# Performance work log

Hardware: AMD Instinct MI355X
Metric: run time of the kernel (lower is better)

Reference implementation:

```python
import jax, jax.numpy as jnp
import numpy as np

B, Q, V, H = 8, 128, 512, 512


def setup_inputs() -> dict:
    key = jax.random.key(0)
    ks = jax.random.split(key, 6)
    s = 1.0 / np.sqrt(H)
    return {
        "query": jax.random.normal(ks[0], (B, Q, H), jnp.float32),
        "values": jax.random.normal(ks[1], (B, V, H), jnp.float32),
        "mask": jax.random.randint(ks[2], (B, V), 0, 2, jnp.int32),
        "Wq": jax.random.normal(ks[3], (H, H), jnp.float32) * s,
        "bq": jnp.zeros((H,), jnp.float32),
        "Wv": jax.random.normal(ks[4], (H, H), jnp.float32) * s,
        "bv": jnp.zeros((H,), jnp.float32),
        "wc": jax.random.normal(ks[5], (H, 1), jnp.float32) * s,
        "bc": jnp.zeros((1,), jnp.float32),
    }


def reference(query, values, mask, Wq, bq, Wv, bv, wc, bc):
    # Project once per token (Q*H and V*H GEMMs), then broadcast-add:
    # faithful to tanh(Lq(q)[:, :, None] + Lv(v)[:, None]) since Linear is
    # applied along the last dim and broadcasting commutes with it.
    qp = jnp.einsum('bqh,kh->bqk', query, Wq) + bq          # [B,Q,H]
    vp = jnp.einsum('bvh,kh->bvk', values, Wv) + bv          # [B,V,H]
    added = jnp.tanh(qp[:, :, None, :] + vp[:, None, :, :])  # [B,Q,V,H]
    scores = jnp.einsum('bqvh,ho->bqv', added, wc) + bc[0]   # [B,Q,V]
    neg_inf = jnp.array(-jnp.inf, scores.dtype)
    scores = jnp.where(mask[:, None, :] == 0, neg_inf, scores)
    weights = jax.nn.softmax(scores, axis=-1)                # [B,Q,V]
    context = jnp.einsum('bqv,bvh->bqh', weights, values)    # [B,Q,H]
    return (context, weights)
```

## Files before the change

### kernel.cpp

```cpp
#include <hip/hip_runtime.h>
#include <hip/hip_bf16.h>


#define C_SCALE 2.8853900817779268f

typedef __attribute__((ext_vector_type(8))) short short8;
typedef __attribute__((ext_vector_type(4))) float f32x4;
typedef __attribute__((ext_vector_type(2))) float f32x2;

__device__ __forceinline__ float fexp2(float x) { return __builtin_amdgcn_exp2f(x); }
__device__ __forceinline__ float frcp(float x)  { return __builtin_amdgcn_rcpf(x); }

__device__ __forceinline__ void bf_split(float x, short& hi, short& lo) {
  unsigned u = __builtin_bit_cast(unsigned, x);
  unsigned r = u + 0x7fffu + ((u >> 16) & 1u);
  hi = (short)(r >> 16);
  float hf = __builtin_bit_cast(float, r & 0xffff0000u);
  lo = (short)(__builtin_bit_cast(unsigned, x - hf) >> 16);
}

__global__ __launch_bounds__(256) void proj_gemm_mfma(
    const float* __restrict__ query, const float* __restrict__ values,
    const float* __restrict__ Wq, const float* __restrict__ Wv,
    const float* __restrict__ bq, const float* __restrict__ bv,
    float* __restrict__ qp, float* __restrict__ vp)
{
  __shared__ short sAhi[64 * 72];
  __shared__ short sAlo[64 * 72];
  __shared__ short sWhi[64 * 72];
  __shared__ short sWlo[64 * 72];

  const int t    = threadIdx.x;
  const int lane = t & 63;
  const int w    = t >> 6;
  const int by   = blockIdx.y;
  const bool isQ = (by < 16);
  const float* A    = isQ ? query : values;
  const float* W    = isQ ? Wq : Wv;
  const float* bias = isQ ? bq : bv;
  float*       out  = isQ ? qp : vp;
  const int m0 = (isQ ? by : (by - 16)) << 6;
  const int n0 = blockIdx.x << 6;

  const int srow = t >> 2, scol = t & 3;
  const float* Ap = A + (size_t)(m0 + srow) * 512 + (scol << 2);
  const float* Wp = W + (size_t)(n0 + srow) * 512 + (scol << 2);

  const int mw = (w & 1) << 5, nw = (w >> 1) << 5;
  const int frow = lane & 15, fquad = lane >> 4;

  f32x4 acc[2][2] = {};
  float4 pfA[4], pfW[4];
#pragma unroll
  for (int p = 0; p < 4; ++p) {
    pfA[p] = *(const float4*)(Ap + (p << 4));
    pfW[p] = *(const float4*)(Wp + (p << 4));
  }

  for (int kc = 0; kc < 512; kc += 64) {
    __syncthreads();
#pragma unroll
    for (int p = 0; p < 4; ++p) {
      float av[4] = {pfA[p].x, pfA[p].y, pfA[p].z, pfA[p].w};
      float wv[4] = {pfW[p].x, pfW[p].y, pfW[p].z, pfW[p].w};
      short4 ah, al, wh, wl;
      short* ahp = (short*)&ah; short* alp = (short*)&al;
      short* whp = (short*)&wh; short* wlp = (short*)&wl;
#pragma unroll
      for (int k = 0; k < 4; ++k) {
        bf_split(av[k], ahp[k], alp[k]);
        bf_split(wv[k], whp[k], wlp[k]);
      }
      const int ofs = srow * 72 + ((p << 2) + scol) * 4;
      *(short4*)&sAhi[ofs] = ah; *(short4*)&sAlo[ofs] = al;
      *(short4*)&sWhi[ofs] = wh; *(short4*)&sWlo[ofs] = wl;
    }
    __syncthreads();
    if (kc + 64 < 512) {
#pragma unroll
      for (int p = 0; p < 4; ++p) {
        pfA[p] = *(const float4*)(Ap + kc + 64 + (p << 4));
        pfW[p] = *(const float4*)(Wp + kc + 64 + (p << 4));
      }
    }
#pragma unroll
    for (int kb = 0; kb < 2; ++kb) {
      const int ko = kb * 32 + fquad * 8;
      short8 ahi[2], alo[2], whi[2], wlo[2];
#pragma unroll
      for (int mt = 0; mt < 2; ++mt) {
        const int r = (mw + mt * 16 + frow) * 72 + ko;
        ahi[mt] = *(const short8*)&sAhi[r];
        alo[mt] = *(const short8*)&sAlo[r];
      }
#pragma unroll
      for (int nt = 0; nt < 2; ++nt) {
        const int r = (nw + nt * 16 + frow) * 72 + ko;
        whi[nt] = *(const short8*)&sWhi[r];
        wlo[nt] = *(const short8*)&sWlo[r];
      }
#pragma unroll
      for (int mt = 0; mt < 2; ++mt)
#pragma unroll
        for (int nt = 0; nt < 2; ++nt) {
          acc[mt][nt] = __builtin_amdgcn_mfma_f32_16x16x32_bf16(
              alo[mt], whi[nt], acc[mt][nt], 0, 0, 0);
          acc[mt][nt] = __builtin_amdgcn_mfma_f32_16x16x32_bf16(
              ahi[mt], wlo[nt], acc[mt][nt], 0, 0, 0);
          acc[mt][nt] = __builtin_amdgcn_mfma_f32_16x16x32_bf16(
              ahi[mt], whi[nt], acc[mt][nt], 0, 0, 0);
        }
    }
  }

#pragma unroll
  for (int nt = 0; nt < 2; ++nt) {
    const int n = n0 + nw + nt * 16 + frow;
    const float bn = bias[n];
#pragma unroll
    for (int mt = 0; mt < 2; ++mt) {
      float vreg[4] = {acc[mt][nt].x, acc[mt][nt].y, acc[mt][nt].z, acc[mt][nt].w};
#pragma unroll
      for (int r = 0; r < 4; ++r) {
        const int m = m0 + mw + mt * 16 + fquad * 4 + r;
        out[(size_t)m * 512 + n] = fexp2(C_SCALE * (vreg[r] + bn));
      }
    }
  }
}

template<int NU>
__device__ __forceinline__ void score_chunkC(
    const float* __restrict__ vpb,
    const f32x2 (&Eq0a)[8][2], const f32x2 (&Eq1a)[8][2], const f32x2 (&wca)[8][2],
    const int* idxs, float* __restrict__ ow0,
    int s00, int i0, int hi, int c4, int lane)
{
  int su[NU];
  unsigned voff[NU];
  f32x2 a0[NU], a1[NU];
#pragma unroll
  for (int u = 0; u < NU; ++u) {
    su[u] = s00 + ((i0 + u) << 4);
    voff[u] = ((unsigned)idxs[su[u] & 511] << 9) + (unsigned)c4;
    a0[u] = (f32x2){0.f, 0.f}; a1[u] = (f32x2){0.f, 0.f};
  }
  const f32x2 one2 = {1.f, 1.f};
#pragma unroll
  for (int j = 0; j < 8; ++j) {
    float4 vv[NU];
#pragma unroll
    for (int u = 0; u < NU; ++u)
      vv[u] = *(const float4*)(vpb + voff[u] + (unsigned)(j << 6));
#pragma unroll
    for (int u = 0; u < NU; ++u) {
      const f32x2 Ev[2] = {{vv[u].x, vv[u].y}, {vv[u].z, vv[u].w}};
#pragma unroll
      for (int kp = 0; kp < 2; ++kp) {
        f32x2 e0 = Ev[kp] * Eq0a[j][kp];
        f32x2 e1 = Ev[kp] * Eq1a[j][kp];
        f32x2 d0 = e0 + one2;
        f32x2 d1 = e1 + one2;
        f32x2 pr = d0 * d1;
        f32x2 P  = {frcp(pr.x), frcp(pr.y)};
        a0[u] = __builtin_elementwise_fma(wca[j][kp] * d1, P, a0[u]);
        a1[u] = __builtin_elementwise_fma(wca[j][kp] * d0, P, a1[u]);
      }
    }
  }
#pragma unroll
  for (int u = 0; u < NU; ++u) {
    float s0 = a0[u].x + a0[u].y;
    float s1 = a1[u].x + a1[u].y;
#pragma unroll
    for (int off = 1; off < 16; off <<= 1) {
      s0 += __shfl_xor(s0, off, 64);
      s1 += __shfl_xor(s1, off, 64);
    }
    if (su[u] < hi && (lane & 15) == (i0 + u)) {
      ow0[su[u]]       = s0;
      ow0[512 + su[u]] = s1;
    }
  }
}

__global__ __launch_bounds__(256) void attn_score(
    const float* __restrict__ qp, const float* __restrict__ vp,
    const int* __restrict__ mask, const float* __restrict__ wc,
    float* __restrict__ out_w)
{
  __shared__ int idxs[512];
  __shared__ int cnt8[8];

  const int t    = threadIdx.x;
  const int lane = t & 63;
  const int w    = t >> 6;
  const int b    = blockIdx.x & 7;
  const int qg   = blockIdx.x >> 3;
  const int rowbase = b * 128 + qg * 2;

  idxs[t] = 0; idxs[t + 256] = 0;
  const int mv0 = mask[b * 512 + t];
  const int mv1 = mask[b * 512 + 256 + t];
  const unsigned long long bal0 = __ballot(mv0 != 0);
  const unsigned long long bal1 = __ballot(mv1 != 0);
  if (lane == 0) { cnt8[w] = __popcll(bal0); cnt8[w + 4] = __popcll(bal1); }
  __syncthreads();
  int cnt = 0, off0 = 0, off4 = 0;
#pragma unroll
  for (int j = 0; j < 8; ++j) {
    if (j == w)     off0 = cnt;
    if (j == w + 4) off4 = cnt;
    cnt += cnt8[j];
  }
  if (mv0) idxs[off0 + __popcll(bal0 & ((1ull << lane) - 1ull))] = t;
  if (mv1) idxs[off4 + __popcll(bal1 & ((1ull << lane) - 1ull))] = t + 256;
  __syncthreads();

  const int c  = blockIdx.y;
  const int lo = (cnt * c) >> 2;
  const int hi = (cnt * (c + 1)) >> 2;
  const int NI = (hi - lo + 15) >> 4;
  const int g  = lane >> 4;
  const int c4 = (lane & 15) << 2;
  const int s00 = lo + (w << 2) + g;

  const float* vpb = vp + (size_t)b * 512 * 512;
  const float* qr0 = qp + (size_t)rowbase * 512;
  float* ow0 = out_w + (size_t)rowbase * 512;

  f32x2 Eq0a[8][2], Eq1a[8][2], wca[8][2];
#pragma unroll
  for (int j = 0; j < 8; ++j) {
    const int hoff = (j << 6) + c4;
    const float4 q0v = *(const float4*)(qr0 + hoff);
    const float4 q1v = *(const float4*)(qr0 + 512 + hoff);
    const float4 wcv = *(const float4*)(wc + hoff);
    Eq0a[j][0] = (f32x2){q0v.x, q0v.y}; Eq0a[j][1] = (f32x2){q0v.z, q0v.w};
    Eq1a[j][0] = (f32x2){q1v.x, q1v.y}; Eq1a[j][1] = (f32x2){q1v.z, q1v.w};
    wca[j][0]  = (f32x2){wcv.x, wcv.y}; wca[j][1]  = (f32x2){wcv.z, wcv.w};
  }

  int i0 = 0;
  for (; i0 + 4 <= NI; i0 += 4)
    score_chunkC<4>(vpb, Eq0a, Eq1a, wca, idxs, ow0, s00, i0, hi, c4, lane);
  for (; i0 < NI; ++i0)
    score_chunkC<1>(vpb, Eq0a, Eq1a, wca, idxs, ow0, s00, i0, hi, c4, lane);
}

__global__ __launch_bounds__(512) void attn_finish(
    const float* __restrict__ values, const int* __restrict__ mask,
    float* __restrict__ out_ctx, float* __restrict__ out_w)
{
  __shared__ int   idxs[512];
  __shared__ float wls2[512][2];
  __shared__ int   cnt8[8];

  const int t    = threadIdx.x;
  const int lane = t & 63;
  const int w    = t >> 6;
  const int b    = blockIdx.x & 7;
  const int qg   = blockIdx.x >> 3;
  const int rowbase = b * 128 + qg * 2;

  ((float*)wls2)[t]       = 0.f;
  ((float*)wls2)[t + 512] = 0.f;
  idxs[t] = 0;
  const int mv = mask[b * 512 + t];
  const unsigned long long bal = __ballot(mv != 0);
  if (lane == 0) cnt8[w] = __popcll(bal);
  __syncthreads();
  int cnt = 0, offw = 0;
#pragma unroll
  for (int j = 0; j < 8; ++j) { if (j == w) offw = cnt; cnt += cnt8[j]; }
  int iinv = -1;
  if (mv) {
    iinv = offw + __popcll(bal & ((1ull << lane) - 1ull));
    idxs[iinv] = t;
  }
  __syncthreads();

  {
    const int mq = (w >= 4) ? 1 : 0;
    const float* srow = out_w + (size_t)(rowbase + mq) * 512;
    float4 u0 = ((const float4*)srow)[lane * 2];
    float4 u1 = ((const float4*)srow)[lane * 2 + 1];
    float s8[8] = {u0.x, u0.y, u0.z, u0.w, u1.x, u1.y, u1.z, u1.w};
#pragma unroll
    for (int k = 0; k < 8; ++k)
      if (lane * 8 + k >= cnt) s8[k] = 3.4e38f;
    float m = s8[0];
#pragma unroll
    for (int k = 1; k < 8; ++k) m = fminf(m, s8[k]);
#pragma unroll
    for (int off = 1; off < 64; off <<= 1) m = fminf(m, __shfl_xor(m, off, 64));
    float e[8], S = 0.f;
#pragma unroll
    for (int k = 0; k < 8; ++k) { e[k] = fexp2(C_SCALE * (m - s8[k])); S += e[k]; }
#pragma unroll
    for (int off = 1; off < 64; off <<= 1) S += __shfl_xor(S, off, 64);
    const float rinv = frcp(S);
    if (w == 0 || w == 4) {
#pragma unroll
      for (int k = 0; k < 8; ++k) {
        const int s = lane * 8 + k;
        if (s < cnt) wls2[s][mq] = e[k] * rinv;
      }
    }
  }
  __syncthreads();

  {
    float w0 = 0.f, w1 = 0.f;
    if (iinv >= 0) { w0 = wls2[iinv][0]; w1 = wls2[iinv][1]; }
    out_w[(size_t)rowbase * 512 + t]       = w0;
    out_w[(size_t)(rowbase + 1) * 512 + t] = w1;
  }

  const int NC = (cnt + 3) >> 2;
  const int g  = lane >> 4;
  const int c4 = (lane & 15) << 2;
  const unsigned hbase = (unsigned)(w * 64 + c4);
  const float* vb = values + (size_t)b * 512 * 512;
  float c0[4] = {0.f, 0.f, 0.f, 0.f}, c1[4] = {0.f, 0.f, 0.f, 0.f};
#pragma unroll 4
  for (int i = 0; i < NC; ++i) {
    const int s = (i << 2) + g;
    const unsigned ro = ((unsigned)idxs[s] << 9) + hbase;
    const float2 wg = *(const float2*)&wls2[s][0];
    const float4 v4 = *(const float4*)(vb + ro);
    float vv[4] = {v4.x, v4.y, v4.z, v4.w};
#pragma unroll
    for (int k = 0; k < 4; ++k) {
      c0[k] = __builtin_fmaf(wg.x, vv[k], c0[k]);
      c1[k] = __builtin_fmaf(wg.y, vv[k], c1[k]);
    }
  }
#pragma unroll
  for (int k = 0; k < 4; ++k) {
    c0[k] += __shfl_xor(c0[k], 16, 64); c0[k] += __shfl_xor(c0[k], 32, 64);
    c1[k] += __shfl_xor(c1[k], 16, 64); c1[k] += __shfl_xor(c1[k], 32, 64);
  }
  if (lane < 16) {
    float4 o0 = {c0[0], c0[1], c0[2], c0[3]};
    float4 o1 = {c1[0], c1[1], c1[2], c1[3]};
    *(float4*)(out_ctx + (size_t)rowbase * 512 + w * 64 + lane * 4)       = o0;
    *(float4*)(out_ctx + (size_t)(rowbase + 1) * 512 + w * 64 + lane * 4) = o1;
  }
}

extern "C" void kernel_launch(void* const* d_in, const int* in_sizes, int n_in,
                              void* d_out, int out_size, void* d_ws, size_t ws_size,
                              hipStream_t stream) {
  const float* query  = (const float*)d_in[0];
  const float* values = (const float*)d_in[1];
  const int*   mask   = (const int*)d_in[2];
  const float* Wq     = (const float*)d_in[3];
  const float* bq     = (const float*)d_in[4];
  const float* Wv     = (const float*)d_in[5];
  const float* bv     = (const float*)d_in[6];
  const float* wc     = (const float*)d_in[7];

  float* out   = (float*)d_out;
  float* out_w = out + (size_t)8 * 128 * 512;
  float* qp    = (float*)d_ws;
  float* vp    = qp + (size_t)1024 * 512;

  proj_gemm_mfma<<<dim3(8, 80), 256, 0, stream>>>(query, values, Wq, Wv, bq, bv, qp, vp);
  attn_score<<<dim3(512, 4), 256, 0, stream>>>(qp, vp, mask, wc, out_w);
  attn_finish<<<512, 512, 0, stream>>>(values, mask, out, out_w);
}
```

Measured before the change: 137.1 us.

## Fuse softmax/context finish into score kernel via last-block atomic counter

After: 323.3 us. 136% more time.

```diff
diff --git a/kernel.cpp b/kernel.cpp
--- a/kernel.cpp
+++ b/kernel.cpp
@@ -23,7 +23,8 @@
     const float* __restrict__ query, const float* __restrict__ values,
     const float* __restrict__ Wq, const float* __restrict__ Wv,
     const float* __restrict__ bq, const float* __restrict__ bv,
-    float* __restrict__ qp, float* __restrict__ vp)
+    float* __restrict__ qp, float* __restrict__ vp,
+    float* __restrict__ out_ctx)
 {
   __shared__ short sAhi[64 * 72];
   __shared__ short sAlo[64 * 72];
@@ -34,6 +35,16 @@
   const int lane = t & 63;
   const int w    = t >> 6;
   const int by   = blockIdx.y;
+
+  if (blockIdx.x == 0 && by == 0) {
+#pragma unroll
+    for (int i = 0; i < 2; ++i) {
+      const int q = t + i * 256;
+      const int bb = q >> 6, qg = q & 63;
+      ((int*)out_ctx)[(size_t)(bb * 128 + qg * 2) * 512] = 0;
+    }
+  }
+
   const bool isQ = (by < 16);
   const float* A    = isQ ? query : values;
   const float* W    = isQ ? Wq : Wv;
@@ -184,13 +195,16 @@
   }
 }
 
-__global__ __launch_bounds__(256) void attn_score(
+__global__ __launch_bounds__(256) void attn_score_finish(
     const float* __restrict__ qp, const float* __restrict__ vp,
-    const int* __restrict__ mask, const float* __restrict__ wc,
-    float* __restrict__ out_w)
+    const float* __restrict__ values, const int* __restrict__ mask,
+    const float* __restrict__ wc,
+    float* __restrict__ out_ctx, float* __restrict__ out_w)
 {
-  __shared__ int idxs[512];
-  __shared__ int cnt8[8];
+  __shared__ int   idxs[512];
+  __shared__ int   cnt8[8];
+  __shared__ float wls2[512][2];
+  __shared__ int   isLast;
 
   const int t    = threadIdx.x;
   const int lane = t & 63;
@@ -199,6 +213,10 @@
   const int qg   = blockIdx.x >> 3;
   const int rowbase = b * 128 + qg * 2;
 
+  ((float*)wls2)[t]       = 0.f;
+  ((float*)wls2)[t + 256] = 0.f;
+  ((float*)wls2)[t + 512] = 0.f;
+  ((float*)wls2)[t + 768] = 0.f;
   idxs[t] = 0; idxs[t + 256] = 0;
   const int mv0 = mask[b * 512 + t];
   const int mv1 = mask[b * 512 + 256 + t];
@@ -213,8 +231,9 @@
     if (j == w + 4) off4 = cnt;
     cnt += cnt8[j];
   }
-  if (mv0) idxs[off0 + __popcll(bal0 & ((1ull << lane) - 1ull))] = t;
-  if (mv1) idxs[off4 + __popcll(bal1 & ((1ull << lane) - 1ull))] = t + 256;
+  int iinv0 = -1, iinv1 = -1;
+  if (mv0) { iinv0 = off0 + __popcll(bal0 & ((1ull << lane) - 1ull)); idxs[iinv0] = t; }
+  if (mv1) { iinv1 = off4 + __popcll(bal1 & ((1ull << lane) - 1ull)); idxs[iinv1] = t + 256; }
   __syncthreads();
 
   const int c  = blockIdx.y;
@@ -246,42 +265,19 @@
     score_chunkC<4>(vpb, Eq0a, Eq1a, wca, idxs, ow0, s00, i0, hi, c4, lane);
   for (; i0 < NI; ++i0)
     score_chunkC<1>(vpb, Eq0a, Eq1a, wca, idxs, ow0, s00, i0, hi, c4, lane);
-}
-
-__global__ __launch_bounds__(512) void attn_finish(
-    const float* __restrict__ values, const int* __restrict__ mask,
-    float* __restrict__ out_ctx, float* __restrict__ out_w)
-{
-  __shared__ int   idxs[512];
-  __shared__ float wls2[512][2];
-  __shared__ int   cnt8[8];
-
-  const int t    = threadIdx.x;
-  const int lane = t & 63;
-  const int w    = t >> 6;
-  const int b    = blockIdx.x & 7;
-  const int qg   = blockIdx.x >> 3;
-  const int rowbase = b * 128 + qg * 2;
-
-  ((float*)wls2)[t]       = 0.f;
-  ((float*)wls2)[t + 512] = 0.f;
-  idxs[t] = 0;
-  const int mv = mask[b * 512 + t];
-  const unsigned long long bal = __ballot(mv != 0);
-  if (lane == 0) cnt8[w] = __popcll(bal);
-  __syncthreads();
-  int cnt = 0, offw = 0;
-#pragma unroll
-  for (int j = 0; j < 8; ++j) { if (j == w) offw = cnt; cnt += cnt8[j]; }
-  int iinv = -1;
-  if (mv) {
-    iinv = offw + __popcll(bal & ((1ull << lane) - 1ull));
-    idxs[iinv] = t;
-  }
-  __syncthreads();
+
+  __threadfence();
+  __syncthreads();
+  if (t == 0) {
+    int old = atomicAdd((int*)(out_ctx + (size_t)rowbase * 512), 1);
+    isLast = (old == 3) ? 1 : 0;
+  }
+  __syncthreads();
+  if (!isLast) return;
+  __threadfence();
 
   {
-    const int mq = (w >= 4) ? 1 : 0;
+    const int mq = w >> 1;
     const float* srow = out_w + (size_t)(rowbase + mq) * 512;
     float4 u0 = ((const float4*)srow)[lane * 2];
     float4 u1 = ((const float4*)srow)[lane * 2 + 1];
@@ -300,7 +296,7 @@
 #pragma unroll
     for (int off = 1; off < 64; off <<= 1) S += __shfl_xor(S, off, 64);
     const float rinv = frcp(S);
-    if (w == 0 || w == 4) {
+    if (w == 0 || w == 2) {
 #pragma unroll
       for (int k = 0; k < 8; ++k) {
         const int s = lane * 8 + k;
@@ -311,41 +307,55 @@
   __syncthreads();
 
   {
-    float w0 = 0.f, w1 = 0.f;
-    if (iinv >= 0) { w0 = wls2[iinv][0]; w1 = wls2[iinv][1]; }
-    out_w[(size_t)rowbase * 512 + t]       = w0;
-    out_w[(size_t)(rowbase + 1) * 512 + t] = w1;
+    float w00 = iinv0 >= 0 ? wls2[iinv0][0] : 0.f;
+    float w01 = iinv0 >= 0 ? wls2[iinv0][1] : 0.f;
+    float w10 = iinv1 >= 0 ? wls2[iinv1][0] : 0.f;
+    float w11 = iinv1 >= 0 ? wls2[iinv1][1] : 0.f;
+    out_w[(size_t)rowbase * 512 + t]             = w00;
+    out_w[(size_t)(rowbase + 1) * 512 + t]       = w01;
+    out_w[(size_t)rowbase * 512 + 256 + t]       = w10;
+    out_w[(size_t)(rowbase + 1) * 512 + 256 + t] = w11;
   }
 
   const int NC = (cnt + 3) >> 2;
-  const int g  = lane >> 4;
-  const int c4 = (lane & 15) << 2;
-  const unsigned hbase = (unsigned)(w * 64 + c4);
+  const unsigned hb0 = (unsigned)(w * 128 + c4);
   const float* vb = values + (size_t)b * 512 * 512;
-  float c0[4] = {0.f, 0.f, 0.f, 0.f}, c1[4] = {0.f, 0.f, 0.f, 0.f};
+  float c00[4] = {}, c01[4] = {}, c10[4] = {}, c11[4] = {};
 #pragma unroll 4
   for (int i = 0; i < NC; ++i) {
     const int s = (i << 2) + g;
-    const unsigned ro = ((unsigned)idxs[s] << 9) + hbase;
+    const unsigned ro = ((unsigned)idxs[s] << 9);
     const float2 wg = *(const float2*)&wls2[s][0];
-    const float4 v4 = *(const float4*)(vb + ro);
-    float vv[4] = {v4.x, v4.y, v4.z, v4.w};
+    const float4 v0 = *(const float4*)(vb + ro + hb0);
+    const float4 v1 = *(const float4*)(vb + ro + hb0 + 64);
+    const float a0[4] = {v0.x, v0.y, v0.z, v0.w};
+    const float a1[4] = {v1.x, v1.y, v1.z, v1.w};
 #pragma unroll
     for (int k = 0; k < 4; ++k) {
-      c0[k] = __builtin_fmaf(wg.x, vv[k], c0[k]);
-      c1[k] = __builtin_fmaf(wg.y, vv[k], c1[k]);
+      c00[k] = __builtin_fmaf(wg.x, a0[k], c00[k]);
+      c01[k] = __builtin_fmaf(wg.x, a1[k], c01[k]);
+      c10[k] = __builtin_fmaf(wg.y, a0[k], c10[k]);
+      c11[k] = __builtin_fmaf(wg.y, a1[k], c11[k]);
     }
   }
 #pragma unroll
   for (int k = 0; k < 4; ++k) {
-    c0[k] += __shfl_xor(c0[k], 16, 64); c0[k] += __shfl_xor(c0[k], 32, 64);
-    c1[k] += __shfl_xor(c1[k], 16, 64); c1[k] += __shfl_xor(c1[k], 32, 64);
+    c00[k] += __shfl_xor(c00[k], 16, 64); c00[k] += __shfl_xor(c00[k], 32, 64);
+    c01[k] += __shfl_xor(c01[k], 16, 64); c01[k] += __shfl_xor(c01[k], 32, 64);
+    c10[k] += __shfl_xor(c10[k], 16, 64); c10[k] += __shfl_xor(c10[k], 32, 64);
+    c11[k] += __shfl_xor(c11[k], 16, 64); c11[k] += __shfl_xor(c11[k], 32, 64);
   }
   if (lane < 16) {
-    float4 o0 = {c0[0], c0[1], c0[2], c0[3]};
-    float4 o1 = {c1[0], c1[1], c1[2], c1[3]};
-    *(float4*)(out_ctx + (size_t)rowbase * 512 + w * 64 + lane * 4)       = o0;
-    *(float4*)(out_ctx + (size_t)(rowbase + 1) * 512 + w * 64 + lane * 4) = o1;
+    float4 o00 = {c00[0], c00[1], c00[2], c00[3]};
+    float4 o01 = {c01[0], c01[1], c01[2], c01[3]};
+    float4 o10 = {c10[0], c10[1], c10[2], c10[3]};
+    float4 o11 = {c11[0], c11[1], c11[2], c11[3]};
+    float* r0 = out_ctx + (size_t)rowbase * 512;
+    float* r1 = out_ctx + (size_t)(rowbase + 1) * 512;
+    *(float4*)(r0 + hb0)      = o00;
+    *(float4*)(r0 + hb0 + 64) = o01;
+    *(float4*)(r1 + hb0)      = o10;
+    *(float4*)(r1 + hb0 + 64) = o11;
   }
 }
 
@@ -366,7 +376,8 @@
   float* qp    = (float*)d_ws;
   float* vp    = qp + (size_t)1024 * 512;
 
-  proj_gemm_mfma<<<dim3(8, 80), 256, 0, stream>>>(query, values, Wq, Wv, bq, bv, qp, vp);
-  attn_score<<<dim3(512, 4), 256, 0, stream>>>(qp, vp, mask, wc, out_w);
-  attn_finish<<<512, 512, 0, stream>>>(values, mask, out, out_w);
-}
+  proj_gemm_mfma<<<dim3(8, 80), 256, 0, stream>>>(query, values, Wq, Wv, bq, bv,
+                                                  qp, vp, out);
+  attn_score_finish<<<dim3(512, 4), 256, 0, stream>>>(qp, vp, values, mask, wc,
+                                                      out, out_w);
+}
```

## Pre-split projection inputs into bf16 hi/lo planes in a separate kernel

Applied to the files above, without the earlier changes.

After: 140.0 us. 2.1% more time.

```diff
diff --git a/kernel.cpp b/kernel.cpp
--- a/kernel.cpp
+++ b/kernel.cpp
@@ -17,6 +17,150 @@
   hi = (short)(r >> 16);
   float hf = __builtin_bit_cast(float, r & 0xffff0000u);
   lo = (short)(__builtin_bit_cast(unsigned, x - hf) >> 16);
+}
+
+__global__ __launch_bounds__(256) void presplit(
+    const float* __restrict__ query, const float* __restrict__ values,
+    const float* __restrict__ Wq, const float* __restrict__ Wv,
+    short* __restrict__ Ahi, short* __restrict__ Alo,
+    short* __restrict__ Whi, short* __restrict__ Wlo)
+{
+  const size_t oct = (size_t)blockIdx.x * 256 + threadIdx.x;
+  const float* src; short *dhi, *dlo;
+  if (oct < 65536) {
+    size_t o = oct * 8;
+    src = query + o; dhi = Ahi + o; dlo = Alo + o;
+  } else if (oct < 327680) {
+    size_t o = (oct - 65536) * 8;
+    src = values + o;
+    dhi = Ahi + (size_t)1024 * 512 + o; dlo = Alo + (size_t)1024 * 512 + o;
+  } else if (oct < 360448) {
+    size_t o = (oct - 327680) * 8;
+    src = Wq + o; dhi = Whi + o; dlo = Wlo + o;
+  } else {
+    size_t o = (oct - 360448) * 8;
+    src = Wv + o;
+    dhi = Whi + (size_t)512 * 512 + o; dlo = Wlo + (size_t)512 * 512 + o;
+  }
+  float4 v0 = *(const float4*)src;
+  float4 v1 = *(const float4*)(src + 4);
+  const float f[8] = {v0.x, v0.y, v0.z, v0.w, v1.x, v1.y, v1.z, v1.w};
+  short8 h, l;
+  short* hp = (short*)&h; short* lp = (short*)&l;
+#pragma unroll
+  for (int k = 0; k < 8; ++k) bf_split(f[k], hp[k], lp[k]);
+  *(short8*)dhi = h;
+  *(short8*)dlo = l;
+}
+
+__global__ __launch_bounds__(256) void proj_gemm_pre(
+    const short* __restrict__ Ahi, const short* __restrict__ Alo,
+    const short* __restrict__ Whi, const short* __restrict__ Wlo,
+    const float* __restrict__ bq, const float* __restrict__ bv,
+    float* __restrict__ qp, float* __restrict__ vp)
+{
+  __shared__ short sAhi[64 * 72];
+  __shared__ short sAlo[64 * 72];
+  __shared__ short sWhi[64 * 72];
+  __shared__ short sWlo[64 * 72];
+
+  const int t    = threadIdx.x;
+  const int lane = t & 63;
+  const int w    = t >> 6;
+  const int by   = blockIdx.y;
+  const bool isQ = (by < 16);
+  const float* bias = isQ ? bq : bv;
+  float*       out  = isQ ? qp : vp;
+  const int m0 = (isQ ? by : (by - 16)) << 6;
+  const int n0 = blockIdx.x << 6;
+  const int arow0 = isQ ? m0 : 1024 + m0;
+  const int wrow0 = isQ ? n0 : 512 + n0;
+
+  const int srow = t >> 2, c16 = (t & 3) << 4;
+  const short* ApH = Ahi + (size_t)(arow0 + srow) * 512 + c16;
+  const short* ApL = Alo + (size_t)(arow0 + srow) * 512 + c16;
+  const short* WpH = Whi + (size_t)(wrow0 + srow) * 512 + c16;
+  const short* WpL = Wlo + (size_t)(wrow0 + srow) * 512 + c16;
+
+  const int mw = (w & 1) << 5, nw = (w >> 1) << 5;
+  const int frow = lane & 15, fquad = lane >> 4;
+
+  f32x4 acc[2][2] = {};
+  short8 pAh[2], pAl[2], pWh[2], pWl[2];
+#pragma unroll
+  for (int p = 0; p < 2; ++p) {
+    pAh[p] = *(const short8*)(ApH + p * 8);
+    pAl[p] = *(const short8*)(ApL + p * 8);
+    pWh[p] = *(const short8*)(WpH + p * 8);
+    pWl[p] = *(const short8*)(WpL + p * 8);
+  }
+
+  for (int kc = 0; kc < 512; kc += 64) {
+    __syncthreads();
+    {
+      const int ofs = srow * 72 + c16;
+#pragma unroll
+      for (int p = 0; p < 2; ++p) {
+        *(short8*)&sAhi[ofs + p * 8] = pAh[p];
+        *(short8*)&sAlo[ofs + p * 8] = pAl[p];
+        *(short8*)&sWhi[ofs + p * 8] = pWh[p];
+        *(short8*)&sWlo[ofs + p * 8] = pWl[p];
+      }
+    }
+    __syncthreads();
+    if (kc + 64 < 512) {
+#pragma unroll
+      for (int p = 0; p < 2; ++p) {
+        pAh[p] = *(const short8*)(ApH + kc + 64 + p * 8);
+        pAl[p] = *(const short8*)(ApL + kc + 64 + p * 8);
+        pWh[p] = *(const short8*)(WpH + kc + 64 + p * 8);
+        pWl[p] = *(const short8*)(WpL + kc + 64 + p * 8);
+      }
+    }
+#pragma unroll
+    for (int kb = 0; kb < 2; ++kb) {
+      const int ko = kb * 32 + fquad * 8;
+      short8 ahi[2], alo[2], whi[2], wlo[2];
+#pragma unroll
+      for (int mt = 0; mt < 2; ++mt) {
+        const int r = (mw + mt * 16 + frow) * 72 + ko;
+        ahi[mt] = *(const short8*)&sAhi[r];
+        alo[mt] = *(const short8*)&sAlo[r];
+      }
+#pragma unroll
+      for (int nt = 0; nt < 2; ++nt) {
+        const int r = (nw + nt * 16 + frow) * 72 + ko;
+        whi[nt] = *(const short8*)&sWhi[r];
+        wlo[nt] = *(const short8*)&sWlo[r];
+      }
+#pragma unroll
+      for (int mt = 0; mt < 2; ++mt)
+#pragma unroll
+        for (int nt = 0; nt < 2; ++nt) {
+          acc[mt][nt] = __builtin_amdgcn_mfma_f32_16x16x32_bf16(
+              alo[mt], whi[nt], acc[mt][nt], 0, 0, 0);
+          acc[mt][nt] = __builtin_amdgcn_mfma_f32_16x16x32_bf16(
+              ahi[mt], wlo[nt], acc[mt][nt], 0, 0, 0);
+          acc[mt][nt] = __builtin_amdgcn_mfma_f32_16x16x32_bf16(
+              ahi[mt], whi[nt], acc[mt][nt], 0, 0, 0);
+        }
+    }
+  }
+
+#pragma unroll
+  for (int nt = 0; nt < 2; ++nt) {
+    const int n = n0 + nw + nt * 16 + frow;
+    const float bn = bias[n];
+#pragma unroll
+    for (int mt = 0; mt < 2; ++mt) {
+      float vreg[4] = {acc[mt][nt].x, acc[mt][nt].y, acc[mt][nt].z, acc[mt][nt].w};
+#pragma unroll
+      for (int r = 0; r < 4; ++r) {
+        const int m = m0 + mw + mt * 16 + fquad * 4 + r;
+        out[(size_t)m * 512 + n] = fexp2(C_SCALE * (vreg[r] + bn));
+      }
+    }
+  }
 }
 
 __global__ __launch_bounds__(256) void proj_gemm_mfma(
@@ -366,7 +510,21 @@
   float* qp    = (float*)d_ws;
   float* vp    = qp + (size_t)1024 * 512;
 
-  proj_gemm_mfma<<<dim3(8, 80), 256, 0, stream>>>(query, values, Wq, Wv, bq, bv, qp, vp);
+  const size_t base   = (size_t)(1024 + 4096) * 512;
+  const size_t needed = base * 4  +
+                        ((size_t)5120 * 512 * 2 + (size_t)1024 * 512 * 2) * 2;
+  if (ws_size >= needed) {
+    short* Ahi = (short*)(vp + (size_t)4096 * 512);
+    short* Alo = Ahi + (size_t)5120 * 512;
+    short* Whi = Alo + (size_t)5120 * 512;
+    short* Wlo = Whi + (size_t)1024 * 512;
+    presplit<<<1536, 256, 0, stream>>>(query, values, Wq, Wv, Ahi, Alo, Whi, Wlo);
+    proj_gemm_pre<<<dim3(8, 80), 256, 0, stream>>>(Ahi, Alo, Whi, Wlo,
+                                                   bq, bv, qp, vp);
+  } else {
+    proj_gemm_mfma<<<dim3(8, 80), 256, 0, stream>>>(query, values, Wq, Wv,
+                                                    bq, bv, qp, vp);
+  }
   attn_score<<<dim3(512, 4), 256, 0, stream>>>(qp, vp, mask, wc, out_w);
   attn_finish<<<512, 512, 0, stream>>>(values, mask, out, out_w);
 }
```
